# Performance work log

Measured on AMD Instinct MI355X. Metric: run time of the kernel, lower is better.

Reference implementation:

```python
import jax, jax.numpy as jnp
import numpy as np

D, N, L, H, VOCAB = 256, 8192, 6, 4, 256
EPS = 1e-5


def layernorm(x):
    # LayerNorm over last dim, no affine (matches nn.LayerNorm(D, elementwise_affine=False))
    mu = jnp.mean(x, axis=-1, keepdims=True)
    var = jnp.mean(jnp.square(x - mu), axis=-1, keepdims=True)
    return (x - mu) * jax.lax.rsqrt(var + EPS)


def rotate_half(x):
    x1, x2 = jnp.split(x, 2, axis=-1)
    return jnp.concatenate((-x2, x1), axis=-1)


def rope_tables(T, dim, dtype):
    inv_freq = 1.0 / (10000.0 ** (jnp.arange(0, dim, 2, dtype=jnp.float32) / dim))
    t = jnp.arange(T, dtype=jnp.float32)
    freqs = jnp.einsum('i,j->ij', t, inv_freq)          # [T, dim/2]
    emb = jnp.concatenate((freqs, freqs), axis=-1)       # [T, dim]
    return jnp.cos(emb).astype(dtype), jnp.sin(emb).astype(dtype)


def linear_attention(Q, K, V):
    # unnormalized causal attention with RoPE on Q, K
    B, T, d = Q.shape
    cos, sin = rope_tables(T, d, Q.dtype)
    Qr = Q * cos + rotate_half(Q) * sin
    Kr = K * cos + rotate_half(K) * sin
    energy = jnp.einsum('btd,bsd->bts', Qr, Kr)          # [B, T, T]
    mask = jnp.tril(jnp.ones((T, T), dtype=energy.dtype))
    energy = energy * mask
    return jnp.einsum('bts,bsd->btd', energy, V)


def setup_inputs() -> dict:
    key = jax.random.key(0)
    ks = jax.random.split(key, 6)
    idx = jax.random.randint(ks[0], (4, 2048), 0, VOCAB)
    wte = jax.random.normal(ks[1], (VOCAB, D), dtype=jnp.float32) * 0.02
    encoder = jax.random.normal(ks[2], (N, D), dtype=jnp.float32) * 0.02
    decoder_x = jax.random.normal(ks[3], (H, D, N // H), dtype=jnp.float32) * 0.02
    decoder_y = jax.random.normal(ks[4], (H, D, N // H), dtype=jnp.float32) * 0.02
    readout = jax.random.normal(ks[5], (D, VOCAB), dtype=jnp.float32) * 0.02
    return {"idx": idx, "wte": wte, "encoder": encoder,
            "decoder_x": decoder_x, "decoder_y": decoder_y, "readout": readout}


def reference(idx, wte, encoder, decoder_x, decoder_y, readout):
    B, T = idx.shape
    v_ast = layernorm(wte[idx])                          # [B, T, D]
    for _ in range(L):
        x_raw = jnp.einsum('btd,hdm->bthm', v_ast, decoder_x)
        x = jax.nn.relu(x_raw)                           # [B, T, H, N/H]
        a_ast = linear_attention(v_ast, v_ast, v_ast)
        y_raw = jnp.einsum('btd,hdm->bthm', layernorm(a_ast), decoder_y)
        y = jax.nn.relu(y_raw) * x
        y_flat = y.reshape(B, T, -1)                     # [B, T, N]
        update = y_flat @ encoder                        # [B, T, D]
        v_ast = v_ast + layernorm(update)
    logits = v_ast @ readout                             # [B, T, VOCAB]
    return logits
```

## Files before the change

kernel.cpp:

```cpp
#include <hip/hip_runtime.h>
#include <hip/hip_bf16.h>

typedef __hip_bfloat16 bf16;
typedef _Float16 half_t;
typedef __attribute__((ext_vector_type(8))) _Float16 half8;
typedef __attribute__((ext_vector_type(4))) float f32x4;

#define LN_EPS 1e-5f

static constexpr int Dk     = 256;
static constexpr int Tk     = 2048;
static constexpr int BTk    = 8192;
static constexpr int MHk    = 2048;
static constexpr int Nk     = 8192;
static constexpr int LAYERS = 6;
static constexpr long long TD  = (long long)Tk * Dk;
static constexpr long long BTD = (long long)BTk * Dk;
static constexpr long long TT  = (long long)Tk * Tk;

#define SKQ(t) ((((t) & 3) ^ (((t) >> 3) & 3)) * 8)

__device__ __forceinline__ float wave_reduce(float v) {
#pragma unroll
    for (int o = 32; o > 0; o >>= 1) v += __shfl_down(v, o);
    return v;
}

__device__ __forceinline__ float block_sum_256(float x, float* sbuf) {
    float s = wave_reduce(x);
    int lane = threadIdx.x & 63, wv = threadIdx.x >> 6;
    if (lane == 0) sbuf[wv] = s;
    __syncthreads();
    float r = sbuf[0] + sbuf[1] + sbuf[2] + sbuf[3];
    __syncthreads();
    return r;
}

__device__ __forceinline__ void glds16(const void* g, void* lds) {
    __builtin_amdgcn_global_load_lds(
        (const __attribute__((address_space(1))) void*)g,
        (__attribute__((address_space(3))) void*)lds, 16, 0, 0);
}

__device__ __forceinline__ void rope_row(const float* nv, int t, half_t* qrow) {
    int i = threadIdx.x;
    if (i < 128) {
        float invf = powf(10000.f, -(float)i / 128.f);
        float ang = (float)t * invf;
        float s, c;
        sincosf(ang, &s, &c);
        float q1 = nv[i], q2 = nv[128 + i];
        qrow[i]       = (half_t)(q1 * c - q2 * s);
        qrow[128 + i] = (half_t)(q2 * c + q1 * s);
    }
}

__global__ __launch_bounds__(256) void sniff_kernel(const unsigned short* __restrict__ w,
                                                    int* __restrict__ flag) {
    __shared__ float sbuf[4];
    int tid = threadIdx.x;
    float cnt = 0.f;
    for (int i = tid; i < 1024; i += 256) {
        int e = (w[i] >> 7) & 0xFF;
        if (e >= 128) cnt += 1.f;
    }
    float tot = block_sum_256(cnt, sbuf);
    if (tid == 0) *flag = (tot > 32.f) ? 1 : 0;
}

__global__ __launch_bounds__(256) void tr_cvt16_kernel(const void* __restrict__ src,
                                                       const int* __restrict__ flag,
                                                       half_t* __restrict__ dst,
                                                       int R, int C,
                                                       long long sz, long long dz) {
    __shared__ float t[32][33];
    bool f32 = (*flag != 0);
    int ct = blockIdx.x * 32, rt = blockIdx.y * 32;
    long long so = (long long)blockIdx.z * sz, dofs = (long long)blockIdx.z * dz;
    int tx = threadIdx.x & 31, ty = threadIdx.x >> 5;
#pragma unroll
    for (int i = 0; i < 4; i++) {
        long long idx = so + (long long)(rt + ty + i * 8) * C + ct + tx;
        t[ty + i * 8][tx] = f32 ? ((const float*)src)[idx] : (float)((const bf16*)src)[idx];
    }
    __syncthreads();
#pragma unroll
    for (int i = 0; i < 4; i++) {
        long long odx = dofs + (long long)(ct + ty + i * 8) * R + rt + tx;
        dst[odx] = (half_t)t[tx][ty + i * 8];
    }
}

__global__ __launch_bounds__(256) void trv_kernel(const float* __restrict__ src,
                                                  half_t* __restrict__ dst) {
    __shared__ float t[32][33];
    int ct = blockIdx.x * 32, rt = blockIdx.y * 32;
    int tx = threadIdx.x & 31, ty = threadIdx.x >> 5;
#pragma unroll
    for (int i = 0; i < 4; i++)
        t[ty + i * 8][tx] = src[(long long)(rt + ty + i * 8) * Dk + ct + tx];
    __syncthreads();
#pragma unroll
    for (int i = 0; i < 4; i++)
        dst[(long long)(ct + ty + i * 8) * BTk + rt + tx] = (half_t)t[tx][ty + i * 8];
}

__global__ __launch_bounds__(256) void embed_ln_kernel(const int* __restrict__ idx,
                                                       const void* __restrict__ wte,
                                                       const int* __restrict__ flag,
                                                       float* __restrict__ v,
                                                       half_t* __restrict__ vf,
                                                       half_t* __restrict__ qf) {
    __shared__ float sbuf[4];
    __shared__ float nvs[256];
    int bt = blockIdx.x, tid = threadIdx.x;
    int id = idx[bt];
    bool f32 = (*flag != 0);
    float x = f32 ? ((const float*)wte)[id * Dk + tid]
                  : (float)((const bf16*)wte)[id * Dk + tid];
    float mu = block_sum_256(x, sbuf) * (1.f / 256.f);
    float d = x - mu;
    float var = block_sum_256(d * d, sbuf) * (1.f / 256.f);
    float r = d * rsqrtf(var + LN_EPS);
    v[bt * Dk + tid] = r;
    vf[bt * Dk + tid] = (half_t)r;
    nvs[tid] = r;
    __syncthreads();
    rope_row(nvs, bt & (Tk - 1), qf + (long long)bt * Dk);
}

__global__ __launch_bounds__(256) void ln_rows_kernel(const float* __restrict__ Pa,
                                                      half_t* __restrict__ of) {
    __shared__ float sbuf[4];
    int bt = blockIdx.x, tid = threadIdx.x;
    int b = bt >> 11, t = bt & (Tk - 1);
    int ncnt = ((t & ~127) >> 9) + 1;
    const float* p = Pa + ((long long)(b << 2)) * TD + (long long)t * Dk + tid;
    float x = 0.f;
    for (int c = 0; c < ncnt; c++) x += p[(long long)c * TD];
    float mu = block_sum_256(x, sbuf) * (1.f / 256.f);
    float d = x - mu;
    float var = block_sum_256(d * d, sbuf) * (1.f / 256.f);
    float r = d * rsqrtf(var + LN_EPS);
    of[bt * Dk + tid] = (half_t)r;
}

__global__ __launch_bounds__(256) void add_ln_kernel(const float* __restrict__ Pu,
                                                     float* __restrict__ v,
                                                     half_t* __restrict__ vf,
                                                     half_t* __restrict__ qf) {
    __shared__ float sbuf[4];
    __shared__ float nvs[256];
    int bt = blockIdx.x, tid = threadIdx.x;
    long long e = (long long)bt * Dk + tid;
    float x = Pu[e] + Pu[e + BTD] + Pu[e + 2 * BTD] + Pu[e + 3 * BTD];
    float mu = block_sum_256(x, sbuf) * (1.f / 256.f);
    float d = x - mu;
    float var = block_sum_256(d * d, sbuf) * (1.f / 256.f);
    float r = d * rsqrtf(var + LN_EPS);
    float nv = v[e] + r;
    v[e] = nv;
    vf[e] = (half_t)nv;
    nvs[tid] = nv;
    __syncthreads();
    rope_row(nvs, bt & (Tk - 1), qf + (long long)bt * Dk);
}

__global__ __launch_bounds__(256) void gemm128e(
    const half_t* __restrict__ Q, half_t* __restrict__ E) {
    __shared__ __align__(16) half_t As[128 * 32];
    __shared__ __align__(16) half_t Bs[128 * 32];
    const int tid = threadIdx.x;
    const int lane = tid & 63, wv = tid >> 6;
    const int wr = wv >> 1, wc = wv & 1;
    const int quad = lane >> 4, r = lane & 15;
    const int qsw = (quad ^ ((r >> 1) & 3)) * 8;
    const int mb = blockIdx.y * 128, nb = blockIdx.x * 128;
    if ((int)blockIdx.x > (int)blockIdx.y) return;
    const half_t* Qb = Q + (long long)blockIdx.z * TD;
    half_t* Eb = E + (long long)blockIdx.z * TT;

    f32x4 acc[4][4] = {};
    const int srow = tid >> 2, skq = SKQ(tid);
    const int wbase = (tid & 192) * 8;
    for (int k0 = 0; k0 < Dk; k0 += 32) {
#pragma unroll
        for (int rnd = 0; rnd < 2; rnd++) {
            int row = rnd * 64 + srow;
            glds16(Qb + (long long)(mb + row) * Dk + k0 + skq, As + rnd * 2048 + wbase);
            glds16(Qb + (long long)(nb + row) * Dk + k0 + skq, Bs + rnd * 2048 + wbase);
        }
        __syncthreads();
        half8 bfr[4];
#pragma unroll
        for (int ni = 0; ni < 4; ni++)
            bfr[ni] = *(const half8*)&Bs[(wc * 64 + ni * 16 + r) * 32 + qsw];
#pragma unroll
        for (int mi = 0; mi < 4; mi++) {
            half8 afr = *(const half8*)&As[(wr * 64 + mi * 16 + r) * 32 + qsw];
#pragma unroll
            for (int ni = 0; ni < 4; ni++)
                acc[mi][ni] = __builtin_amdgcn_mfma_f32_16x16x32_f16(afr, bfr[ni], acc[mi][ni], 0, 0, 0);
        }
        __syncthreads();
    }
#pragma unroll
    for (int mi = 0; mi < 4; mi++)
#pragma unroll
        for (int ni = 0; ni < 4; ni++) {
            int row0 = mb + wr * 64 + mi * 16 + quad * 4;
            int col = nb + wc * 64 + ni * 16 + r;
#pragma unroll
            for (int rr = 0; rr < 4; rr++) {
                int row = row0 + rr;
                float val = (row < col) ? 0.f : acc[mi][ni][rr];
                Eb[(long long)row * Tk + col] = (half_t)val;
            }
        }
}

__global__ __launch_bounds__(256) void gemm128a(
    const half_t* __restrict__ E, const half_t* __restrict__ vT,
    float* __restrict__ Pa) {
    __shared__ __align__(16) half_t As[128 * 32];
    __shared__ __align__(16) half_t Bs[128 * 32];
    const int tid = threadIdx.x;
    const int lane = tid & 63, wv = tid >> 6;
    const int wr = wv >> 1, wc = wv & 1;
    const int quad = lane >> 4, r = lane & 15;
    const int qsw = (quad ^ ((r >> 1) & 3)) * 8;
    const int mb = blockIdx.x * 128, nb = blockIdx.y * 128;
    const int b = blockIdx.z >> 2, c = blockIdx.z & 3;
    const int kbeg = c * 512;
    const int kend = min(mb + 128, kbeg + 512);
    if (kend <= kbeg) return;

    const half_t* Ab = E + (long long)b * TT;
    const half_t* Bb = vT + (long long)b * Tk;
    float* Pc = Pa + (long long)blockIdx.z * TD;
    f32x4 acc[4][4] = {};
    const int srow = tid >> 2, skq = SKQ(tid);
    const int wbase = (tid & 192) * 8;
    for (int k0 = kbeg; k0 < kend; k0 += 32) {
#pragma unroll
        for (int rnd = 0; rnd < 2; rnd++) {
            int row = rnd * 64 + srow;
            glds16(Ab + (long long)(mb + row) * Tk + k0 + skq, As + rnd * 2048 + wbase);
            glds16(Bb + (long long)(nb + row) * BTk + k0 + skq, Bs + rnd * 2048 + wbase);
        }
        __syncthreads();
        half8 bfr[4];
#pragma unroll
        for (int ni = 0; ni < 4; ni++)
            bfr[ni] = *(const half8*)&Bs[(wc * 64 + ni * 16 + r) * 32 + qsw];
#pragma unroll
        for (int mi = 0; mi < 4; mi++) {
            half8 afr = *(const half8*)&As[(wr * 64 + mi * 16 + r) * 32 + qsw];
#pragma unroll
            for (int ni = 0; ni < 4; ni++)
                acc[mi][ni] = __builtin_amdgcn_mfma_f32_16x16x32_f16(afr, bfr[ni], acc[mi][ni], 0, 0, 0);
        }
        __syncthreads();
    }
#pragma unroll
    for (int mi = 0; mi < 4; mi++)
#pragma unroll
        for (int ni = 0; ni < 4; ni++) {
            int row0 = mb + wr * 64 + mi * 16 + quad * 4;
            int col = nb + wc * 64 + ni * 16 + r;
#pragma unroll
            for (int rr = 0; rr < 4; rr++)
                Pc[(long long)(row0 + rr) * Dk + col] = acc[mi][ni][rr];
        }
}

__global__ __launch_bounds__(256, 1) void dual_update(
    const half_t* __restrict__ A1,
    const half_t* __restrict__ A2,
    const half_t* __restrict__ dxT,
    const half_t* __restrict__ dyT,
    const half_t* __restrict__ eT,
    float* __restrict__ Pu) {
    __shared__ __align__(16) half_t smem[32768];
    half_t* As1 = smem;
    half_t* As2 = smem + 8192;
    half_t* Bs1 = smem + 16384;
    half_t* Bs2 = smem + 24576;
    half_t* yld = smem;
    half_t* eTs = smem + 16384;

    const int tid = threadIdx.x;
    const int lane = tid & 63, wv = tid >> 6;
    const int wr = wv >> 1, wc = wv & 1;
    const int quad = lane >> 4, r = lane & 15;
    const int qsw = (quad ^ ((r >> 1) & 3)) * 8;
    const int xcd = blockIdx.x & 7, j = blockIdx.x >> 3;
    const int mt = xcd * 8 + (j & 7);
    const int h = j >> 3;
    const int mb = mt * 128;
    const half_t* B1 = dxT + (long long)h * MHk * Dk;
    const half_t* B2 = dyT + (long long)h * MHk * Dk;
    const half_t* Eh = eT + (long long)h * MHk;
    float* Pc = Pu + (long long)h * BTD;

    const int srow8 = lane >> 3;
    const int soct  = (lane & 7) ^ srow8;
    const int srow = tid >> 2, skq = SKQ(tid);
    const int wbase = (tid & 192) * 8;

    f32x4 accU[4][8] = {};
    for (int nt = 0; nt < 16; ++nt) {
        const int nb = nt * 128;
        f32x4 accX[4][4] = {};
        f32x4 accY[4][4] = {};
        for (int k0 = 0; k0 < Dk; k0 += 64) {
#pragma unroll
            for (int st = 0; st < 4; st++) {
                int row = wv * 32 + st * 8;
                long long ga = (long long)(mb + row + srow8) * Dk + k0 + soct * 8;
                long long gb = (long long)(nb + row + srow8) * Dk + k0 + soct * 8;
                glds16(A1 + ga, As1 + row * 64);
                glds16(A2 + ga, As2 + row * 64);
                glds16(B1 + gb, Bs1 + row * 64);
                glds16(B2 + gb, Bs2 + row * 64);
            }
            __syncthreads();
#pragma unroll
            for (int sub = 0; sub < 2; sub++) {
                half8 b1f[4], b2f[4];
#pragma unroll
                for (int ni = 0; ni < 4; ni++) {
                    int R = wc * 64 + ni * 16 + r;
                    int pos = ((sub * 4 + quad) ^ (R & 7)) * 8;
                    b1f[ni] = *(const half8*)&Bs1[R * 64 + pos];
                    b2f[ni] = *(const half8*)&Bs2[R * 64 + pos];
                }
#pragma unroll
                for (int mi = 0; mi < 4; mi++) {
                    int R = wr * 64 + mi * 16 + r;
                    int pos = ((sub * 4 + quad) ^ (R & 7)) * 8;
                    half8 a1 = *(const half8*)&As1[R * 64 + pos];
                    half8 a2 = *(const half8*)&As2[R * 64 + pos];
#pragma unroll
                    for (int ni = 0; ni < 4; ni++) {
                        accX[mi][ni] = __builtin_amdgcn_mfma_f32_16x16x32_f16(a1, b1f[ni], accX[mi][ni], 0, 0, 0);
                        accY[mi][ni] = __builtin_amdgcn_mfma_f32_16x16x32_f16(a2, b2f[ni], accY[mi][ni], 0, 0, 0);
                    }
                }
            }
            __syncthreads();
        }
#pragma unroll
        for (int mi = 0; mi < 4; mi++)
#pragma unroll
            for (int ni = 0; ni < 4; ni++) {
                int col = wc * 64 + ni * 16 + r;
                int row0 = wr * 64 + mi * 16 + quad * 4;
#pragma unroll
                for (int rr = 0; rr < 4; rr++) {
                    int W = row0 + rr;
                    float val = fmaxf(accY[mi][ni][rr], 0.f) * fmaxf(accX[mi][ni][rr], 0.f);
                    yld[W * 128 + (((col >> 3) ^ ((W & 12) >> 1)) << 3) + (col & 7)] = (half_t)val;
                }
            }
#pragma unroll
        for (int rnd = 0; rnd < 4; rnd++) {
            int row = rnd * 64 + srow;
            glds16(Eh + (long long)row * Nk + nb + skq, eTs + rnd * 2048 + wbase);
        }
        __syncthreads();
#pragma unroll
        for (int c = 0; c < 4; ++c) {
            if (c < 3) {
#pragma unroll
                for (int rnd = 0; rnd < 4; rnd++) {
                    int row = rnd * 64 + srow;
                    glds16(Eh + (long long)row * Nk + nb + (c + 1) * 32 + skq,
                           eTs + ((c + 1) & 1) * 8192 + rnd * 2048 + wbase);
                }
            }
            half8 bu[8];
#pragma unroll
            for (int ni = 0; ni < 8; ni++)
                bu[ni] = *(const half8*)&eTs[(c & 1) * 8192 + (wc * 128 + ni * 16 + r) * 32 + qsw];
#pragma unroll
            for (int mi = 0; mi < 4; mi++) {
                int R = wr * 64 + mi * 16 + r;
                half8 au = *(const half8*)&yld[R * 128 + ((((c << 2) + quad) ^ ((R & 12) >> 1)) << 3)];
#pragma unroll
                for (int ni = 0; ni < 8; ni++)
                    accU[mi][ni] = __builtin_amdgcn_mfma_f32_16x16x32_f16(au, bu[ni], accU[mi][ni], 0, 0, 0);
            }
            __syncthreads();
        }
    }
#pragma unroll
    for (int mi = 0; mi < 4; mi++)
#pragma unroll
        for (int ni = 0; ni < 8; ni++) {
            int row0 = mb + wr * 64 + mi * 16 + quad * 4;
            int col = wc * 128 + ni * 16 + r;
#pragma unroll
            for (int rr = 0; rr < 4; rr++)
                Pc[(long long)(row0 + rr) * Dk + col] = accU[mi][ni][rr];
        }
}

__global__ __launch_bounds__(256) void gemm64h(
    const half_t* __restrict__ A, int lda,
    const half_t* __restrict__ B, int ldb,
    float* __restrict__ C, int ldc, int K) {
    __shared__ __align__(16) half_t As[64 * 32];
    __shared__ __align__(16) half_t Bs[64 * 32];
    const int tid = threadIdx.x;
    const int lane = tid & 63, wv = tid >> 6;
    const int wr = wv >> 1, wc = wv & 1;
    const int quad = lane >> 4, r = lane & 15;
    const int qsw = (quad ^ ((r >> 1) & 3)) * 8;
    const int mb = blockIdx.y * 64, nb = blockIdx.x * 64;

    f32x4 acc[2][2] = {};
    const int srow = tid >> 2, skq = SKQ(tid);
    const int wbase = (tid & 192) * 8;
    for (int k0 = 0; k0 < K; k0 += 32) {
        glds16(A + (long long)(mb + srow) * lda + k0 + skq, As + wbase);
        glds16(B + (long long)(nb + srow) * ldb + k0 + skq, Bs + wbase);
        __syncthreads();
        half8 b0 = *(const half8*)&Bs[(wc * 32 +  0 + r) * 32 + qsw];
        half8 b1 = *(const half8*)&Bs[(wc * 32 + 16 + r) * 32 + qsw];
#pragma unroll
        for (int mi = 0; mi < 2; mi++) {
            half8 afr = *(const half8*)&As[(wr * 32 + mi * 16 + r) * 32 + qsw];
            acc[mi][0] = __builtin_amdgcn_mfma_f32_16x16x32_f16(afr, b0, acc[mi][0], 0, 0, 0);
            acc[mi][1] = __builtin_amdgcn_mfma_f32_16x16x32_f16(afr, b1, acc[mi][1], 0, 0, 0);
        }
        __syncthreads();
    }
#pragma unroll
    for (int mi = 0; mi < 2; mi++)
#pragma unroll
        for (int ni = 0; ni < 2; ni++) {
            int row0 = mb + wr * 32 + mi * 16 + quad * 4;
            int col = nb + wc * 32 + ni * 16 + r;
#pragma unroll
            for (int rr = 0; rr < 4; rr++)
                C[(long long)(row0 + rr) * ldc + col] = acc[mi][ni][rr];
        }
}

extern "C" void kernel_launch(void* const* d_in, const int* in_sizes, int n_in,
                              void* d_out, int out_size, void* d_ws, size_t ws_size,
                              hipStream_t stream) {
    (void)in_sizes; (void)n_in; (void)out_size; (void)ws_size;
    const int* idx = (const int*)d_in[0];
    float* out = (float*)d_out;

    char* ws = (char*)d_ws;
    float*  v32  = (float*) (ws);
    half_t* vf   = (half_t*)(ws + (  8ll << 20));
    half_t* qf   = (half_t*)(ws + ( 12ll << 20));
    half_t* vT   = (half_t*)(ws + ( 16ll << 20));
    half_t* lnf  = (half_t*)(ws + ( 20ll << 20));
    half_t* E    = (half_t*)(ws + ( 24ll << 20));
    float*  Pa   = (float*) (ws + ( 56ll << 20));
    float*  Pu   = (float*) (ws + ( 24ll << 20));
    half_t* dxT  = (half_t*)(ws + (216ll << 20));
    half_t* dyT  = (half_t*)(ws + (220ll << 20));
    half_t* eT   = (half_t*)(ws + (224ll << 20));
    half_t* roT  = (half_t*)(ws + (228ll << 20));
    int*    flag = (int*)   (ws + (228ll << 20) + (256ll << 10));

    sniff_kernel<<<1, 256, 0, stream>>>((const unsigned short*)d_in[1], flag);
    tr_cvt16_kernel<<<dim3(MHk / 32, Dk / 32, 4), 256, 0, stream>>>(
        d_in[3], flag, dxT, Dk, MHk, (long long)Dk * MHk, (long long)Dk * MHk);
    tr_cvt16_kernel<<<dim3(MHk / 32, Dk / 32, 4), 256, 0, stream>>>(
        d_in[4], flag, dyT, Dk, MHk, (long long)Dk * MHk, (long long)Dk * MHk);
    tr_cvt16_kernel<<<dim3(Dk / 32, Nk / 32, 1), 256, 0, stream>>>(
        d_in[2], flag, eT, Nk, Dk, 0, 0);
    tr_cvt16_kernel<<<dim3(Dk / 32, Dk / 32, 1), 256, 0, stream>>>(
        d_in[5], flag, roT, Dk, Dk, 0, 0);

    embed_ln_kernel<<<BTk, 256, 0, stream>>>(idx, d_in[1], flag, v32, vf, qf);

    for (int l = 0; l < LAYERS; l++) {
        trv_kernel<<<dim3(Dk / 32, BTk / 32), 256, 0, stream>>>(v32, vT);
        gemm128e<<<dim3(Tk / 128, Tk / 128, 4), 256, 0, stream>>>(qf, E);
        gemm128a<<<dim3(Tk / 128, Dk / 128, 16), 256, 0, stream>>>(E, vT, Pa);
        ln_rows_kernel<<<BTk, 256, 0, stream>>>(Pa, lnf);
        dual_update<<<dim3(256), 256, 0, stream>>>(vf, lnf, dxT, dyT, eT, Pu);
        add_ln_kernel<<<BTk, 256, 0, stream>>>(Pu, v32, vf, qf);
    }
    gemm64h<<<dim3(Dk / 64, BTk / 64), 256, 0, stream>>>(
        vf, Dk, roT, Dk, out, Dk, Dk);
}
```

Baseline: 1.527 ms.

## Double wave count in dual_update to 8 waves with split tile ownership

Raises dual_update from 4 to 8 waves per block (512 threads). The 2x4 wave grid halves each wave's accumulator tiles, and the global-to-LDS loads are reassigned so each wave pair fills one of the four operand buffers. The LDS swizzle for the intermediate y tile also changes. The aim is more latency hiding and lower register pressure per wave for the dual GEMM plus encoder product. The cost is more barrier participants and changed LDS bank patterns, and with only 256 blocks the grid occupancy stays one block per CU.

```diff
diff --git a/kernel.cpp b/kernel.cpp
--- a/kernel.cpp
+++ b/kernel.cpp
@@ -274,7 +274,7 @@
         }
 }
 
-__global__ __launch_bounds__(256, 1) void dual_update(
+__global__ __launch_bounds__(512, 2) void dual_update(
     const half_t* __restrict__ A1,
     const half_t* __restrict__ A2,
     const half_t* __restrict__ dxT,
@@ -282,18 +282,14 @@
     const half_t* __restrict__ eT,
     float* __restrict__ Pu) {
     __shared__ __align__(16) half_t smem[32768];
-    half_t* As1 = smem;
-    half_t* As2 = smem + 8192;
-    half_t* Bs1 = smem + 16384;
-    half_t* Bs2 = smem + 24576;
     half_t* yld = smem;
     half_t* eTs = smem + 16384;
 
     const int tid = threadIdx.x;
-    const int lane = tid & 63, wv = tid >> 6;
-    const int wr = wv >> 1, wc = wv & 1;
+    const int lane = tid & 63, w = tid >> 6;
+    const int wr = w >> 2, wc = w & 3;
     const int quad = lane >> 4, r = lane & 15;
-    const int qsw = (quad ^ ((r >> 1) & 3)) * 8;
+
     const int xcd = blockIdx.x & 7, j = blockIdx.x >> 3;
     const int mt = xcd * 8 + (j & 7);
     const int h = j >> 3;
@@ -303,46 +299,49 @@
     const half_t* Eh = eT + (long long)h * MHk;
     float* Pc = Pu + (long long)h * BTD;
 
+    const int bufid = w >> 1, halfsel = w & 1;
     const int srow8 = lane >> 3;
-    const int soct  = (lane & 7) ^ srow8;
-    const int srow = tid >> 2, skq = SKQ(tid);
-    const int wbase = (tid & 192) * 8;
-
-    f32x4 accU[4][8] = {};
+    const int soct = (lane & 7) ^ srow8;
+    half_t* sb = smem + bufid * 8192;
+    const bool isA = (bufid < 2);
+    const half_t* gbase = (bufid == 0) ? A1 : (bufid == 1) ? A2
+                        : (bufid == 2) ? B1 : B2;
+
+    const int erow = tid >> 2;
+    const int eskq = SKQ(tid);
+
+    f32x4 accU[4][4] = {};
     for (int nt = 0; nt < 16; ++nt) {
         const int nb = nt * 128;
-        f32x4 accX[4][4] = {};
-        f32x4 accY[4][4] = {};
+        const long long gro = isA ? (long long)mb : (long long)nb;
+        f32x4 accX[4][2] = {};
+        f32x4 accY[4][2] = {};
         for (int k0 = 0; k0 < Dk; k0 += 64) {
 #pragma unroll
-            for (int st = 0; st < 4; st++) {
-                int row = wv * 32 + st * 8;
-                long long ga = (long long)(mb + row + srow8) * Dk + k0 + soct * 8;
-                long long gb = (long long)(nb + row + srow8) * Dk + k0 + soct * 8;
-                glds16(A1 + ga, As1 + row * 64);
-                glds16(A2 + ga, As2 + row * 64);
-                glds16(B1 + gb, Bs1 + row * 64);
-                glds16(B2 + gb, Bs2 + row * 64);
+            for (int t = 0; t < 8; t++) {
+                int row = t * 16 + halfsel * 8;
+                glds16(gbase + (gro + row + srow8) * Dk + k0 + soct * 8,
+                       sb + row * 64);
             }
             __syncthreads();
 #pragma unroll
             for (int sub = 0; sub < 2; sub++) {
-                half8 b1f[4], b2f[4];
-#pragma unroll
-                for (int ni = 0; ni < 4; ni++) {
-                    int R = wc * 64 + ni * 16 + r;
+                half8 b1f[2], b2f[2];
+#pragma unroll
+                for (int ni = 0; ni < 2; ni++) {
+                    int R = wc * 32 + ni * 16 + r;
                     int pos = ((sub * 4 + quad) ^ (R & 7)) * 8;
-                    b1f[ni] = *(const half8*)&Bs1[R * 64 + pos];
-                    b2f[ni] = *(const half8*)&Bs2[R * 64 + pos];
+                    b1f[ni] = *(const half8*)&smem[16384 + R * 64 + pos];
+                    b2f[ni] = *(const half8*)&smem[24576 + R * 64 + pos];
                 }
 #pragma unroll
                 for (int mi = 0; mi < 4; mi++) {
                     int R = wr * 64 + mi * 16 + r;
                     int pos = ((sub * 4 + quad) ^ (R & 7)) * 8;
-                    half8 a1 = *(const half8*)&As1[R * 64 + pos];
-                    half8 a2 = *(const half8*)&As2[R * 64 + pos];
-#pragma unroll
-                    for (int ni = 0; ni < 4; ni++) {
+                    half8 a1 = *(const half8*)&smem[R * 64 + pos];
+                    half8 a2 = *(const half8*)&smem[8192 + R * 64 + pos];
+#pragma unroll
+                    for (int ni = 0; ni < 2; ni++) {
                         accX[mi][ni] = __builtin_amdgcn_mfma_f32_16x16x32_f16(a1, b1f[ni], accX[mi][ni], 0, 0, 0);
                         accY[mi][ni] = __builtin_amdgcn_mfma_f32_16x16x32_f16(a2, b2f[ni], accY[mi][ni], 0, 0, 0);
                     }
@@ -353,42 +352,41 @@
 #pragma unroll
         for (int mi = 0; mi < 4; mi++)
 #pragma unroll
-            for (int ni = 0; ni < 4; ni++) {
-                int col = wc * 64 + ni * 16 + r;
+            for (int ni = 0; ni < 2; ni++) {
+                int col = wc * 32 + ni * 16 + r;
                 int row0 = wr * 64 + mi * 16 + quad * 4;
 #pragma unroll
                 for (int rr = 0; rr < 4; rr++) {
                     int W = row0 + rr;
                     float val = fmaxf(accY[mi][ni][rr], 0.f) * fmaxf(accX[mi][ni][rr], 0.f);
-                    yld[W * 128 + (((col >> 3) ^ ((W & 12) >> 1)) << 3) + (col & 7)] = (half_t)val;
+                    yld[W * 128 + (((col >> 3) ^ (W & 7)) << 3) + (col & 7)] = (half_t)val;
                 }
             }
 #pragma unroll
-        for (int rnd = 0; rnd < 4; rnd++) {
-            int row = rnd * 64 + srow;
-            glds16(Eh + (long long)row * Nk + nb + skq, eTs + rnd * 2048 + wbase);
-        }
+        for (int rd = 0; rd < 2; rd++)
+            glds16(Eh + (long long)(rd * 128 + erow) * Nk + nb + eskq,
+                   eTs + rd * 4096 + w * 512);
         __syncthreads();
 #pragma unroll
         for (int c = 0; c < 4; ++c) {
             if (c < 3) {
 #pragma unroll
-                for (int rnd = 0; rnd < 4; rnd++) {
-                    int row = rnd * 64 + srow;
-                    glds16(Eh + (long long)row * Nk + nb + (c + 1) * 32 + skq,
-                           eTs + ((c + 1) & 1) * 8192 + rnd * 2048 + wbase);
-                }
-            }
-            half8 bu[8];
-#pragma unroll
-            for (int ni = 0; ni < 8; ni++)
-                bu[ni] = *(const half8*)&eTs[(c & 1) * 8192 + (wc * 128 + ni * 16 + r) * 32 + qsw];
+                for (int rd = 0; rd < 2; rd++)
+                    glds16(Eh + (long long)(rd * 128 + erow) * Nk + nb + (c + 1) * 32 + eskq,
+                           eTs + ((c + 1) & 1) * 8192 + rd * 4096 + w * 512);
+            }
+            half8 bu[4];
+#pragma unroll
+            for (int ni = 0; ni < 4; ni++) {
+                int d = wc * 64 + ni * 16 + r;
+                bu[ni] = *(const half8*)&eTs[(c & 1) * 8192 + d * 32 + ((quad ^ ((r >> 1) & 3)) << 3)];
+            }
 #pragma unroll
             for (int mi = 0; mi < 4; mi++) {
                 int R = wr * 64 + mi * 16 + r;
-                half8 au = *(const half8*)&yld[R * 128 + ((((c << 2) + quad) ^ ((R & 12) >> 1)) << 3)];
-#pragma unroll
-                for (int ni = 0; ni < 8; ni++)
+                half8 au = *(const half8*)&yld[R * 128 + (((c * 4 + quad) ^ (R & 7)) << 3)];
+#pragma unroll
+                for (int ni = 0; ni < 4; ni++)
                     accU[mi][ni] = __builtin_amdgcn_mfma_f32_16x16x32_f16(au, bu[ni], accU[mi][ni], 0, 0, 0);
             }
             __syncthreads();
@@ -397,9 +395,9 @@
 #pragma unroll
     for (int mi = 0; mi < 4; mi++)
 #pragma unroll
-        for (int ni = 0; ni < 8; ni++) {
+        for (int ni = 0; ni < 4; ni++) {
             int row0 = mb + wr * 64 + mi * 16 + quad * 4;
-            int col = wc * 128 + ni * 16 + r;
+            int col = wc * 64 + ni * 16 + r;
 #pragma unroll
             for (int rr = 0; rr < 4; rr++)
                 Pc[(long long)(row0 + rr) * Dk + col] = accU[mi][ni][rr];
@@ -487,7 +485,7 @@
         gemm128e<<<dim3(Tk / 128, Tk / 128, 4), 256, 0, stream>>>(qf, E);
         gemm128a<<<dim3(Tk / 128, Dk / 128, 16), 256, 0, stream>>>(E, vT, Pa);
         ln_rows_kernel<<<BTk, 256, 0, stream>>>(Pa, lnf);
-        dual_update<<<dim3(256), 256, 0, stream>>>(vf, lnf, dxT, dyT, eT, Pu);
+        dual_update<<<dim3(256), 512, 0, stream>>>(vf, lnf, dxT, dyT, eT, Pu);
         add_ln_kernel<<<BTk, 256, 0, stream>>>(Pu, v32, vf, qf);
     }
     gemm64h<<<dim3(Dk / 64, BTk / 64), 256, 0, stream>>>(
```

Measured after the change: 1.295 ms. 15.2% less time.
